# Performance work log

Hardware: AMD Instinct MI355X
Metric: run time of the kernel (lower is better)

## Reference

```python
import jax, jax.numpy as jnp
import numpy as np

N = 8192        # nodes in batch
E = 262144      # edges (avg degree 32)
IN_C = 64
OUT_C = 64
K = 3           # max_k
G = 64          # graphs in batch
NC = 10         # n_class
EPS = 1e-5      # batchnorm eps


def setup_inputs() -> dict:
    key = jax.random.key(0)
    ks = jax.random.split(key, 16)
    D_in = IN_C * K    # 192
    D_out = OUT_C * K  # 192
    inp = {
        'x': jax.random.normal(ks[0], (N, IN_C), jnp.float32),
        'edge_index': jax.random.randint(ks[1], (2, E), 0, N, dtype=jnp.int64),
        'batch': jnp.sort(jax.random.randint(ks[2], (N,), 0, G, dtype=jnp.int64)),
        # spectral-normed masked linear
        'W_orig': jax.random.normal(ks[3], (D_out, D_in), jnp.float32) * 0.05,
        'b': jnp.zeros((D_out,), jnp.float32),
        'u': jax.random.normal(ks[4], (D_out,), jnp.float32),
        # batchnorms (training-mode batch stats)
        'bn1_gamma': jnp.ones((D_out,), jnp.float32),
        'bn1_beta': jnp.zeros((D_out,), jnp.float32),
        'bn2_gamma': jnp.ones((D_out * 3,), jnp.float32),
        'bn2_beta': jnp.zeros((D_out * 3,), jnp.float32),
        # funnel head
        'w1': jax.random.normal(ks[5], (D_out * 2, D_out * 3), jnp.float32) * 0.05,
        'b1': jnp.zeros((D_out * 2,), jnp.float32),
        'w2': jax.random.normal(ks[6], (D_out, D_out * 2), jnp.float32) * 0.05,
        'b2': jnp.zeros((D_out,), jnp.float32),
        'w3': jax.random.normal(ks[7], (NC, D_out), jnp.float32) * 0.05,
        'b3': jnp.zeros((NC,), jnp.float32),
    }
    return inp


def _forward(x, edge_index, batch, W_orig, b, u, bn1_gamma, bn1_beta,
             bn2_gamma, bn2_beta, w1, b1, w2, b2, w3, b3):
    n = x.shape[0]
    row, col = edge_index[0], edge_index[1]
    # sym-normalized Laplacian L = I - D^-1/2 A D^-1/2, densified ([N,N])
    deg = jnp.zeros((n,), x.dtype).at[row].add(1.0)
    dinv = jnp.where(deg > 0, jax.lax.rsqrt(jnp.maximum(deg, 1.0)), 0.0)
    vals = -dinv[row] * dinv[col]
    L = jnp.zeros((n, n), x.dtype).at[row, col].add(vals)
    idx = jnp.arange(n)
    L = L.at[idx, idx].add(1.0)
    Hs = [x]
    h = x
    for _ in range(K - 1):
        h = L @ h
        Hs.append(h)
    Hcat = jnp.concatenate(Hs, axis=1)              # [N, IN_C*K]
    # spectral norm of W (one power-iteration step with stored u)
    v = W_orig.T @ u
    v = v / (jnp.linalg.norm(v) + 1e-12)
    sigma = u @ (W_orig @ v)
    W = W_orig / sigma
    # block lower-triangular mask: block i passes first IN_C*(i+1) input cols
    col_idx = jnp.arange(IN_C * K)
    row_block = jnp.arange(OUT_C * K) // OUT_C
    mask = (col_idx[None, :] < IN_C * (row_block[:, None] + 1)).astype(W.dtype)
    H = Hcat @ (W * mask).T + b                     # masked linear
    # reservoir_act_fun is identity (default)
    mu, var = H.mean(0), H.var(0)                   # BN (batch stats)
    H = bn1_gamma * (H - mu) * jax.lax.rsqrt(var + EPS) + bn1_beta
    # fused-style triple pooling over graph ids
    Hsum = jax.ops.segment_sum(H, batch, num_segments=G)
    cnt = jax.ops.segment_sum(jnp.ones((n,), H.dtype), batch, num_segments=G)
    Havg = Hsum / jnp.maximum(cnt, 1.0)[:, None]
    Hmax = jax.ops.segment_max(H, batch, num_segments=G)
    Hg = jnp.concatenate([Havg, Hsum, Hmax], axis=1)  # [G, 3*OUT_C*K]
    mu2, var2 = Hg.mean(0), Hg.var(0)
    xo = bn2_gamma * (Hg - mu2) * jax.lax.rsqrt(var2 + EPS) + bn2_beta
    # funnel output (dropout = identity in eval)
    xo = jax.nn.relu(xo @ w1.T + b1)
    xo = jax.nn.relu(xo @ w2.T + b2)
    return jax.nn.log_softmax(xo @ w3.T + b3, axis=1)


def reference(x, edge_index, batch, W_orig, b, u, bn1_gamma, bn1_beta,
              bn2_gamma, bn2_beta, w1, b1, w2, b2, w3, b3):
    return _forward(x, edge_index, batch, W_orig, b, u, bn1_gamma, bn1_beta,
                    bn2_gamma, bn2_beta, w1, b1, w2, b2, w3, b3)
```

## Files before the change

### kernel.cpp

```cpp
#include <hip/hip_runtime.h>
#include <math.h>

#define NN   8192
#define EE   262144
#define CIN  64
#define DD   192
#define GG   64
#define NCLS 10
#define D3   576
#define F1   384
#define F2   192
#define EPSB 1e-5f
#define NB   64
#define EPB  (EE / NB)

__device__ __forceinline__ unsigned int fkey(float f) {
    unsigned int b = __float_as_uint(f);
    return b ^ (0x80000000u | (unsigned int)((int)b >> 31));
}
__device__ __forceinline__ float fdec(unsigned int k) {
    unsigned int b = k ^ ((k & 0x80000000u) ? 0x80000000u : 0xFFFFFFFFu);
    return __uint_as_float(b);
}

__global__ __launch_bounds__(1024) void prep_kernel(const float* __restrict__ W,
    const float* __restrict__ u, const float* __restrict__ w1,
    const float* __restrict__ w2, const int* __restrict__ batch,
    const int* __restrict__ ei,
    float* __restrict__ sig, int* __restrict__ gstart,
    unsigned short* __restrict__ pcnt,
    float* __restrict__ Wp, float* __restrict__ Wp1, float* __restrict__ Wp2,
    int* __restrict__ pinit) {
    __shared__ int hist[NN];
    int b = blockIdx.x, t = threadIdx.x;
    if (b < 324) {
        int idx = b * 1024 + t;
        if (idx < DD * DD) {
            int r = idx / DD, c = idx - r * DD;
            float m = (c < CIN * ((r >> 6) + 1)) ? 1.f : 0.f;
            Wp[((c >> 2) * DD + r) * 4 + (c & 3)] = m * W[idx];
        } else if (idx < DD * DD + F1 * D3) {
            int i1 = idx - DD * DD;
            int tt = i1 / D3, k = i1 - tt * D3;
            Wp1[((k >> 2) * F1 + tt) * 4 + (k & 3)] = w1[i1];
        } else {
            int i2 = idx - DD * DD - F1 * D3;
            int tt = i2 / F1, k = i2 - tt * F1;
            Wp2[((k >> 2) * F2 + tt) * 4 + (k & 3)] = w2[i2];
        }
        return;
    }
    if (b == 325) {
        for (int i = t; i < NN; i += 1024) {
            int b0 = batch[i];
            int b1 = (i + 1 < NN) ? batch[i + 1] : GG;
            if (i == 0) { for (int g = 0; g <= b0; g++) gstart[g] = 0; }
            for (int g = b0 + 1; g <= b1; g++) gstart[g] = i + 1;
        }
        return;
    }
    if (b == 326 + NB) {
        int4* z = (int4*)pinit;
        for (int i = t; i < 3 * GG * DD / 4; i += 1024) z[i] = make_int4(0, 0, 0, 0);
        int4* m = (int4*)(pinit + 3 * GG * DD);
        for (int i = t; i < GG * DD / 4; i += 1024) m[i] = make_int4(-1, -1, -1, -1);
        return;
    }
    if (b >= 326) {
        int cb = b - 326;
        int4* hz = (int4*)hist;
        for (int i = t; i < NN / 4; i += 1024) hz[i] = make_int4(0, 0, 0, 0);
        __syncthreads();
        int e0 = cb * EPB;
        for (int i = t; i < EPB; i += 1024) atomicAdd(&hist[ei[e0 + i]], 1);
        __syncthreads();
        const int2* h2 = (const int2*)hist;
        ushort2* q2 = (ushort2*)&pcnt[cb * NN];
        for (int i = t; i < NN / 2; i += 1024) {
            int2 h = h2[i];
            q2[i] = make_ushort2((unsigned short)h.x, (unsigned short)h.y);
        }
        return;
    }
    float* vp  = (float*)hist;
    float* vsh = vp + 768;
    float* red = vsh + DD;
    if (t < 768) {
        int c = t >> 2, j = t & 3;
        float s = 0.f;
        const float* Wc = W + c;
        for (int i = j * 48; i < j * 48 + 48; i++) s += Wc[i * DD] * u[i];
        vp[t] = s;
    }
    __syncthreads();
    float vv = 0.f;
    if (t < DD) {
        float v = vp[4 * t] + vp[4 * t + 1] + vp[4 * t + 2] + vp[4 * t + 3];
        vsh[t] = v;
        vv = v * v;
    }
    red[t] = vv;
    __syncthreads();
    for (int off = 512; off > 0; off >>= 1) {
        if (t < off) red[t] += red[t + off];
        __syncthreads();
    }
    float norm = sqrtf(red[0]) + 1e-12f;
    __syncthreads();
    float a = 0.f;
    for (int idx = t; idx < DD * DD; idx += 1024) {
        int r = idx / DD, c = idx - r * DD;
        a += u[r] * W[idx] * vsh[c];
    }
    red[t] = a;
    __syncthreads();
    for (int off = 512; off > 0; off >>= 1) {
        if (t < off) red[t] += red[t + off];
        __syncthreads();
    }
    if (t == 0) sig[0] = norm / red[0];
}

__global__ __launch_bounds__(256) void offs_kernel(unsigned short* __restrict__ pcnt,
                                                   int* __restrict__ deg,
                                                   float* __restrict__ dinv) {
    int i = blockIdx.x * 256 + threadIdx.x;
    int run = 0;
#pragma unroll
    for (int b = 0; b < NB; b++) {
        int v = pcnt[b * NN + i];
        pcnt[b * NN + i] = (unsigned short)run;
        run += v;
    }
    deg[i] = run;
    dinv[i] = (run > 0) ? rsqrtf((float)run) : 0.f;
}

__global__ __launch_bounds__(1024) void scatter_kernel(const int* __restrict__ ei,
                                                       const int* __restrict__ deg,
                                                       const unsigned short* __restrict__ off,
                                                       int* __restrict__ rowptr,
                                                       unsigned short* __restrict__ csr_col) {
    __shared__ int cur[NN];
    __shared__ int temp[1024];
    int b = blockIdx.x, t = threadIdx.x;
    int base = t * 8;
    int d[8], l[8];
    {
        const int4 a4 = *(const int4*)&deg[base];
        const int4 b4 = *(const int4*)&deg[base + 4];
        d[0] = a4.x; d[1] = a4.y; d[2] = a4.z; d[3] = a4.w;
        d[4] = b4.x; d[5] = b4.y; d[6] = b4.z; d[7] = b4.w;
    }
    int run = 0;
#pragma unroll
    for (int j = 0; j < 8; j++) { l[j] = run; run += d[j]; }
    temp[t] = run;
    __syncthreads();
    for (int o = 1; o < 1024; o <<= 1) {
        int v = (t >= o) ? temp[t - o] : 0;
        __syncthreads();
        temp[t] += v;
        __syncthreads();
    }
    int prefix = (t > 0) ? temp[t - 1] : 0;
    {
        const unsigned short* ob = &off[b * NN];
        int4 opk = *(const int4*)(ob + base);
        cur[base + 0] = prefix + l[0] + (opk.x & 0xFFFF);
        cur[base + 1] = prefix + l[1] + (int)((unsigned)opk.x >> 16);
        cur[base + 2] = prefix + l[2] + (opk.y & 0xFFFF);
        cur[base + 3] = prefix + l[3] + (int)((unsigned)opk.y >> 16);
        cur[base + 4] = prefix + l[4] + (opk.z & 0xFFFF);
        cur[base + 5] = prefix + l[5] + (int)((unsigned)opk.z >> 16);
        cur[base + 6] = prefix + l[6] + (opk.w & 0xFFFF);
        cur[base + 7] = prefix + l[7] + (int)((unsigned)opk.w >> 16);
    }
    if (b == 0) {
#pragma unroll
        for (int j = 0; j < 8; j++) rowptr[base + j] = prefix + l[j];
        if (t == 1023) rowptr[NN] = temp[1023];
    }
    __syncthreads();
    int e0 = b * EPB;
    for (int i = t; i < EPB; i += 1024) {
        int r = ei[e0 + i];
        int c = ei[EE + e0 + i];
        int pos = atomicAdd(&cur[r], 1);
        csr_col[pos] = (unsigned short)c;
    }
}

__global__ __launch_bounds__(256) void spmm_kernel(const float* __restrict__ hin,
    int in_stride, int in_off,
    const int* __restrict__ rowptr, const unsigned short* __restrict__ col,
    const float* __restrict__ dinv,
    float* __restrict__ Hcat, int coff, int write_self) {
    int idx = blockIdx.x * 256 + threadIdx.x;
    int row = idx >> 6;
    int lane = idx & 63;
    int s = rowptr[row], e = rowptr[row + 1];
    float acc0 = 0.f, acc1 = 0.f, acc2 = 0.f, acc3 = 0.f;
    int p = s;
    for (; p + 3 < e; p += 4) {
        int c0 = col[p], c1 = col[p + 1], c2 = col[p + 2], c3 = col[p + 3];
        acc0 += dinv[c0] * hin[c0 * in_stride + in_off + lane];
        acc1 += dinv[c1] * hin[c1 * in_stride + in_off + lane];
        acc2 += dinv[c2] * hin[c2 * in_stride + in_off + lane];
        acc3 += dinv[c3] * hin[c3 * in_stride + in_off + lane];
    }
    for (; p < e; p++) {
        int c = col[p];
        acc0 += dinv[c] * hin[c * in_stride + in_off + lane];
    }
    float acc = (acc0 + acc1) + (acc2 + acc3);
    float self = hin[row * in_stride + in_off + lane];
    Hcat[row * DD + coff + lane] = self - dinv[row] * acc;
    if (write_self) Hcat[row * DD + lane] = self;
}

__global__ __launch_bounds__(384) void gemm_pool_kernel(const float* __restrict__ Hcat,
    const float* __restrict__ Wp, const float* __restrict__ bias,
    const float* __restrict__ sig, const int* __restrict__ batch,
    float* __restrict__ Psum, float* __restrict__ Psq,
    unsigned int* __restrict__ Pmaxk, unsigned int* __restrict__ Pmink) {
    __shared__ float hs[16 * DD];
    __shared__ int bb[16];
    int t = threadIdx.x;
    int n0 = blockIdx.x * 16;
    const float4* src = (const float4*)&Hcat[n0 * DD];
    float4* dst = (float4*)hs;
    dst[t] = src[t];
    dst[t + 384] = src[t + 384];
    if (t < 16) bb[t] = batch[n0 + t];
    __syncthreads();
    int half = t / 192;
    int ch = t - half * 192;
    int r0 = half * 8;
    float acc[8];
#pragma unroll
    for (int r = 0; r < 8; r++) acc[r] = 0.f;
    const float4* Wp4 = (const float4*)Wp;
    const float* hb = &hs[r0 * DD];
    for (int k4 = 0; k4 < DD / 4; k4++) {
        float4 w = Wp4[k4 * DD + ch];
#pragma unroll
        for (int r = 0; r < 8; r++) {
            const float4 h = *(const float4*)&hb[r * DD + k4 * 4];
            acc[r] += h.x * w.x + h.y * w.y + h.z * w.z + h.w * w.w;
        }
    }
    float inv_sigma = sig[0];
    float bv = bias[ch];
    int gcur = bb[r0];
    float sum = 0.f, sq = 0.f, mn = INFINITY, mx = -INFINITY;
#pragma unroll
    for (int r = 0; r < 8; r++) {
        float v = inv_sigma * acc[r] + bv;
        int g = bb[r0 + r];
        if (g != gcur) {
            atomicAdd(&Psum[gcur * DD + ch], sum);
            atomicAdd(&Psq[gcur * DD + ch], sq);
            atomicMax(&Pmaxk[gcur * DD + ch], fkey(mx));
            atomicMin(&Pmink[gcur * DD + ch], fkey(mn));
            sum = 0.f; sq = 0.f; mn = INFINITY; mx = -INFINITY; gcur = g;
        }
        sum += v; sq += v * v;
        mn = fminf(mn, v); mx = fmaxf(mx, v);
    }
    atomicAdd(&Psum[gcur * DD + ch], sum);
    atomicAdd(&Psq[gcur * DD + ch], sq);
    atomicMax(&Pmaxk[gcur * DD + ch], fkey(mx));
    atomicMin(&Pmink[gcur * DD + ch], fkey(mn));
}

__global__ __launch_bounds__(64) void hg_kernel(
    const float* __restrict__ Psum, const float* __restrict__ Psq,
    const unsigned int* __restrict__ Pmaxk, const unsigned int* __restrict__ Pmink,
    const int* __restrict__ gstart,
    const float* __restrict__ g1, const float* __restrict__ be1,
    const float* __restrict__ g2, const float* __restrict__ be2,
    float* __restrict__ Hg) {
    int t = blockIdx.x;
    int g = threadIdx.x;
    int f = t / DD, c = t - f * DD;
    float Sg = Psum[g * DD + c];
    float Qg = Psq[g * DD + c];
    float S = Sg, Q = Qg;
    for (int off = 32; off > 0; off >>= 1) {
        S += __shfl_xor(S, off);
        Q += __shfl_xor(Q, off);
    }
    float mu = S * (1.f / (float)NN);
    float var = Q * (1.f / (float)NN) - mu * mu;
    float sc = g1[c] * rsqrtf(var + EPSB);
    float bb = be1[c];
    float v;
    if (f == 2) {
        float mx = fdec(Pmaxk[g * DD + c]);
        float mn = fdec(Pmink[g * DD + c]);
        float raw = (sc >= 0.f) ? mx : mn;
        v = sc * (raw - mu) + bb;
    } else {
        float nf = (float)(gstart[g + 1] - gstart[g]);
        float hsum = sc * (Sg - nf * mu) + nf * bb;
        v = (f == 0) ? hsum / fmaxf(nf, 1.f) : hsum;
    }
    float s2 = v, ss2 = v * v;
    for (int off = 32; off > 0; off >>= 1) {
        s2 += __shfl_xor(s2, off);
        ss2 += __shfl_xor(ss2, off);
    }
    float m2 = s2 * (1.f / (float)GG);
    float var2 = ss2 * (1.f / (float)GG) - m2 * m2;
    float sc2 = g2[t] * rsqrtf(var2 + EPSB);
    Hg[g * D3 + t] = sc2 * (v - m2) + be2[t];
}

__global__ __launch_bounds__(F1) void funnel_kernel(const float* __restrict__ Hg,
    const float* __restrict__ Wp1, const float* __restrict__ b1,
    const float* __restrict__ Wp2, const float* __restrict__ b2,
    const float* __restrict__ w3, const float* __restrict__ b3,
    float* __restrict__ out) {
    __shared__ float hg[D3];
    __shared__ float x1[F1];
    __shared__ float x2[F2];
    __shared__ float lg[NCLS];
    __shared__ float s_lse;
    int g = blockIdx.x, t = threadIdx.x;
    for (int i = t; i < D3; i += F1) hg[i] = Hg[g * D3 + i];
    __syncthreads();
    {
        float a = b1[t];
        const float4* W4 = (const float4*)Wp1;
        for (int k4 = 0; k4 < D3 / 4; k4++) {
            float4 w = W4[k4 * F1 + t];
            const float4 h = *(const float4*)&hg[k4 * 4];
            a += w.x * h.x + w.y * h.y + w.z * h.z + w.w * h.w;
        }
        x1[t] = fmaxf(a, 0.f);
    }
    __syncthreads();
    if (t < F2) {
        float a = b2[t];
        const float4* W4 = (const float4*)Wp2;
        for (int k4 = 0; k4 < F1 / 4; k4++) {
            float4 w = W4[k4 * F2 + t];
            const float4 h = *(const float4*)&x1[k4 * 4];
            a += w.x * h.x + w.y * h.y + w.z * h.z + w.w * h.w;
        }
        x2[t] = fmaxf(a, 0.f);
    }
    __syncthreads();
    if (t < NCLS) {
        float a = b3[t];
        const float4* wr = (const float4*)&w3[t * F2];
        const float4* h4 = (const float4*)x2;
        for (int k = 0; k < F2 / 4; k++) {
            float4 w = wr[k], h = h4[k];
            a += w.x * h.x + w.y * h.y + w.z * h.z + w.w * h.w;
        }
        lg[t] = a;
    }
    __syncthreads();
    if (t == 0) {
        float m = lg[0];
        for (int i = 1; i < NCLS; i++) m = fmaxf(m, lg[i]);
        float se = 0.f;
        for (int i = 0; i < NCLS; i++) se += expf(lg[i] - m);
        s_lse = m + logf(se);
    }
    __syncthreads();
    if (t < NCLS) out[g * NCLS + t] = lg[t] - s_lse;
}


extern "C" void kernel_launch(void* const* d_in, const int* in_sizes, int n_in,
                              void* d_out, int out_size, void* d_ws, size_t ws_size,
                              hipStream_t stream) {
    (void)in_sizes; (void)n_in; (void)out_size; (void)ws_size;
    const float* x     = (const float*)d_in[0];
    const int*   ei    = (const int*)d_in[1];
    const int*   batch = (const int*)d_in[2];
    const float* W     = (const float*)d_in[3];
    const float* b     = (const float*)d_in[4];
    const float* u     = (const float*)d_in[5];
    const float* g1    = (const float*)d_in[6];
    const float* be1   = (const float*)d_in[7];
    const float* g2    = (const float*)d_in[8];
    const float* be2   = (const float*)d_in[9];
    const float* w1    = (const float*)d_in[10];
    const float* b1    = (const float*)d_in[11];
    const float* w2    = (const float*)d_in[12];
    const float* b2    = (const float*)d_in[13];
    const float* w3    = (const float*)d_in[14];
    const float* b3    = (const float*)d_in[15];
    float* out = (float*)d_out;
    char*  ws  = (char*)d_ws;

    int*            gstart  = (int*)(ws + 0);
    int*            rowptr  = (int*)(ws + 512);
    int*            deg     = (int*)(ws + 33536);
    float*          dinv    = (float*)(ws + 66304);
    float*          sig     = (float*)(ws + 99072);
    float*          Wp      = (float*)(ws + 99328);
    float*          Psum    = (float*)(ws + 246784);
    float*          Psq     = (float*)(ws + 295936);
    unsigned int*   Pmaxk   = (unsigned int*)(ws + 345088);
    unsigned int*   Pmink   = (unsigned int*)(ws + 394240);
    float*          Hg      = (float*)(ws + 443392);
    unsigned short* csr_col = (unsigned short*)(ws + 590848);
    float*          Wp1     = (float*)(ws + 1115136);
    float*          Wp2     = (float*)(ws + 1999872);
    unsigned short* pcnt    = (unsigned short*)(ws + 2294784);
    float*          Hcat    = (float*)(ws + 3343360);

    prep_kernel<<<326 + NB + 1, 1024, 0, stream>>>(W, u, w1, w2, batch, ei,
                                                   sig, gstart, pcnt, Wp, Wp1, Wp2,
                                                   (int*)Psum);
    offs_kernel<<<NN / 256, 256, 0, stream>>>(pcnt, deg, dinv);
    scatter_kernel<<<NB, 1024, 0, stream>>>(ei, deg, pcnt, rowptr, csr_col);
    spmm_kernel<<<NN * 64 / 256, 256, 0, stream>>>(x, CIN, 0, rowptr, csr_col, dinv, Hcat, CIN, 1);
    spmm_kernel<<<NN * 64 / 256, 256, 0, stream>>>(Hcat, DD, CIN, rowptr, csr_col, dinv, Hcat, 2 * CIN, 0);
    gemm_pool_kernel<<<NN / 16, 384, 0, stream>>>(Hcat, Wp, b, sig, batch,
                                                  Psum, Psq, Pmaxk, Pmink);
    hg_kernel<<<D3, 64, 0, stream>>>(Psum, Psq, Pmaxk, Pmink, gstart, g1, be1, g2, be2, Hg);
    funnel_kernel<<<GG, F1, 0, stream>>>(Hg, Wp1, b1, Wp2, b2, w3, b3, out);
}
```

Baseline: 181.7 us.

## Fuse second SpMM hop into GEMM+pool kernel and drop Hcat buffer

The second Laplacian hop is now computed inside the GEMM/pooling kernel, writing its result straight into shared memory instead of a global Hcat buffer. The first hop writes a compact 64-wide Hx1 array rather than strided columns of a 192-wide Hcat, so gathers in the second hop read contiguous 256-byte rows. This removes one kernel launch and the global round trip of the concatenated features. In exchange, the GEMM kernel gets a gather phase run by only 6 waves over 16 rows, which may lower gather parallelism and add load imbalance per block.

```diff
diff --git a/kernel.cpp b/kernel.cpp
--- a/kernel.cpp
+++ b/kernel.cpp
@@ -191,11 +191,9 @@
     }
 }
 
-__global__ __launch_bounds__(256) void spmm_kernel(const float* __restrict__ hin,
-    int in_stride, int in_off,
+__global__ __launch_bounds__(256) void spmm1_kernel(const float* __restrict__ x,
     const int* __restrict__ rowptr, const unsigned short* __restrict__ col,
-    const float* __restrict__ dinv,
-    float* __restrict__ Hcat, int coff, int write_self) {
+    const float* __restrict__ dinv, float* __restrict__ Hx1) {
     int idx = blockIdx.x * 256 + threadIdx.x;
     int row = idx >> 6;
     int lane = idx & 63;
@@ -204,22 +202,24 @@
     int p = s;
     for (; p + 3 < e; p += 4) {
         int c0 = col[p], c1 = col[p + 1], c2 = col[p + 2], c3 = col[p + 3];
-        acc0 += dinv[c0] * hin[c0 * in_stride + in_off + lane];
-        acc1 += dinv[c1] * hin[c1 * in_stride + in_off + lane];
-        acc2 += dinv[c2] * hin[c2 * in_stride + in_off + lane];
-        acc3 += dinv[c3] * hin[c3 * in_stride + in_off + lane];
+        acc0 += dinv[c0] * x[c0 * 64 + lane];
+        acc1 += dinv[c1] * x[c1 * 64 + lane];
+        acc2 += dinv[c2] * x[c2 * 64 + lane];
+        acc3 += dinv[c3] * x[c3 * 64 + lane];
     }
     for (; p < e; p++) {
         int c = col[p];
-        acc0 += dinv[c] * hin[c * in_stride + in_off + lane];
+        acc0 += dinv[c] * x[c * 64 + lane];
     }
     float acc = (acc0 + acc1) + (acc2 + acc3);
-    float self = hin[row * in_stride + in_off + lane];
-    Hcat[row * DD + coff + lane] = self - dinv[row] * acc;
-    if (write_self) Hcat[row * DD + lane] = self;
-}
-
-__global__ __launch_bounds__(384) void gemm_pool_kernel(const float* __restrict__ Hcat,
+    float self = x[row * 64 + lane];
+    Hx1[row * 64 + lane] = self - dinv[row] * acc;
+}
+
+__global__ __launch_bounds__(384) void sgp_kernel(const float* __restrict__ x,
+    const float* __restrict__ Hx1,
+    const int* __restrict__ rowptr, const unsigned short* __restrict__ col,
+    const float* __restrict__ dinv,
     const float* __restrict__ Wp, const float* __restrict__ bias,
     const float* __restrict__ sig, const int* __restrict__ batch,
     float* __restrict__ Psum, float* __restrict__ Psq,
@@ -228,11 +228,37 @@
     __shared__ int bb[16];
     int t = threadIdx.x;
     int n0 = blockIdx.x * 16;
-    const float4* src = (const float4*)&Hcat[n0 * DD];
-    float4* dst = (float4*)hs;
-    dst[t] = src[t];
-    dst[t + 384] = src[t + 384];
+    for (int i = t; i < 512; i += 384) {
+        int r = i >> 5, q = i & 31;
+        float4 v = (q < 16) ? ((const float4*)x)[(n0 + r) * 16 + q]
+                            : ((const float4*)Hx1)[(n0 + r) * 16 + (q - 16)];
+        *(float4*)&hs[r * DD + q * 4] = v;
+    }
     if (t < 16) bb[t] = batch[n0 + t];
+    __syncthreads();
+    {
+        int lane = t & 63, wv = t >> 6;
+        for (int r = wv; r < 16; r += 6) {
+            int row = n0 + r;
+            int s = rowptr[row], e = rowptr[row + 1];
+            float acc0 = 0.f, acc1 = 0.f, acc2 = 0.f, acc3 = 0.f;
+            int p = s;
+            for (; p + 3 < e; p += 4) {
+                int c0 = col[p], c1 = col[p + 1], c2 = col[p + 2], c3 = col[p + 3];
+                acc0 += dinv[c0] * Hx1[c0 * 64 + lane];
+                acc1 += dinv[c1] * Hx1[c1 * 64 + lane];
+                acc2 += dinv[c2] * Hx1[c2 * 64 + lane];
+                acc3 += dinv[c3] * Hx1[c3 * 64 + lane];
+            }
+            for (; p < e; p++) {
+                int c = col[p];
+                acc0 += dinv[c] * Hx1[c * 64 + lane];
+            }
+            float acc = (acc0 + acc1) + (acc2 + acc3);
+            float self = hs[r * DD + 64 + lane];
+            hs[r * DD + 128 + lane] = self - dinv[row] * acc;
+        }
+    }
     __syncthreads();
     int half = t / 192;
     int ch = t - half * 192;
@@ -413,17 +439,17 @@
     float*          Wp1     = (float*)(ws + 1115136);
     float*          Wp2     = (float*)(ws + 1999872);
     unsigned short* pcnt    = (unsigned short*)(ws + 2294784);
-    float*          Hcat    = (float*)(ws + 3343360);
+    float*          Hx1     = (float*)(ws + 3343360);
 
     prep_kernel<<<326 + NB + 1, 1024, 0, stream>>>(W, u, w1, w2, batch, ei,
                                                    sig, gstart, pcnt, Wp, Wp1, Wp2,
                                                    (int*)Psum);
     offs_kernel<<<NN / 256, 256, 0, stream>>>(pcnt, deg, dinv);
     scatter_kernel<<<NB, 1024, 0, stream>>>(ei, deg, pcnt, rowptr, csr_col);
-    spmm_kernel<<<NN * 64 / 256, 256, 0, stream>>>(x, CIN, 0, rowptr, csr_col, dinv, Hcat, CIN, 1);
-    spmm_kernel<<<NN * 64 / 256, 256, 0, stream>>>(Hcat, DD, CIN, rowptr, csr_col, dinv, Hcat, 2 * CIN, 0);
-    gemm_pool_kernel<<<NN / 16, 384, 0, stream>>>(Hcat, Wp, b, sig, batch,
-                                                  Psum, Psq, Pmaxk, Pmink);
+    spmm1_kernel<<<NN * 64 / 256, 256, 0, stream>>>(x, rowptr, csr_col, dinv, Hx1);
+    sgp_kernel<<<NN / 16, 384, 0, stream>>>(x, Hx1, rowptr, csr_col, dinv,
+                                            Wp, b, sig, batch,
+                                            Psum, Psq, Pmaxk, Pmink);
     hg_kernel<<<D3, 64, 0, stream>>>(Psum, Psq, Pmaxk, Pmink, gstart, g1, be1, g2, be2, Hg);
     funnel_kernel<<<GG, F1, 0, stream>>>(Hg, Wp1, b1, Wp2, b2, w3, b3, out);
 }
```

Result: no change. 184.7 us (+1.6%).
